# Kernel optimization log

Measured on AMD Instinct MI355X. Metric: run time of the kernel, lower is better.

## Reference

```python
import jax, jax.numpy as jnp
import numpy as np

HEAD_NUM = 16


def setup_inputs() -> dict:
    key = jax.random.key(0)
    ks = jax.random.split(key, 7)
    B, S, D = 4, 2048, 1024
    scale = 1.0 / np.sqrt(D)
    return {
        "q": jax.random.normal(ks[0], (B, S, D), jnp.float32),
        "k": jax.random.normal(ks[1], (B, S, D), jnp.float32),
        "v": jax.random.normal(ks[2], (B, S, D), jnp.float32),
        "w_q": jax.random.normal(ks[3], (D, D), jnp.float32) * scale,
        "w_k": jax.random.normal(ks[4], (D, D), jnp.float32) * scale,
        "w_v": jax.random.normal(ks[5], (D, D), jnp.float32) * scale,
        "w_o": jax.random.normal(ks[6], (D, D), jnp.float32) * scale,
    }


def reference(q, k, v, w_q, w_k, w_v, w_o):
    B, Sq, _ = q.shape
    H = HEAD_NUM
    d_k = w_q.shape[1] // H  # per-head key dim

    def split_heads(x):
        b, s, _ = x.shape
        return x.reshape(b, s, H, -1).transpose(0, 2, 1, 3)  # [b,h,s,d]

    hq = split_heads(q @ w_q)
    hk = split_heads(k @ w_k)
    hv = split_heads(v @ w_v)

    scores = jnp.einsum("bhqd,bhkd->bhqk", hq, hk) / jnp.sqrt(
        jnp.asarray(d_k, dtype=hq.dtype)
    )
    attn = jax.nn.softmax(scores, axis=-1)
    out = jnp.einsum("bhqk,bhkd->bhqd", attn, hv)  # [b,h,q,d]
    out = out.transpose(0, 2, 1, 3).reshape(B, Sq, -1)  # concat heads
    return out @ w_o
```

## Files before the change

kernel.cpp:

```cpp
#include <hip/hip_runtime.h>

typedef unsigned short u16;
typedef short vshort8 __attribute__((ext_vector_type(8)));
typedef __bf16 vbf16x8 __attribute__((ext_vector_type(8)));
typedef float vf32x4 __attribute__((ext_vector_type(4)));
typedef float vf32x16 __attribute__((ext_vector_type(16)));

__device__ __forceinline__ u16 f2bf(float f) {
  unsigned u = __builtin_bit_cast(unsigned, f);
  u += 0x7FFFu + ((u >> 16) & 1u);
  return (u16)(u >> 16);
}

__device__ __forceinline__ unsigned cvtpk(float lo, float hi) {
  unsigned r;
  asm("v_cvt_pk_bf16_f32 %0, %1, %2" : "=v"(r) : "v"(lo), "v"(hi));
  return r;
}

__device__ __forceinline__ void plswap(unsigned& a, unsigned& b) {
  asm("v_permlane32_swap_b32 %0, %1" : "+v"(a), "+v"(b));
}

__device__ __forceinline__ float swap32f(float x) { return __shfl_xor(x, 32); }

__device__ __forceinline__ vf32x4 mfma_bf16(vshort8 a, vshort8 b, vf32x4 c) {
  return __builtin_amdgcn_mfma_f32_16x16x32_bf16(
      __builtin_bit_cast(vbf16x8, a), __builtin_bit_cast(vbf16x8, b), c, 0, 0, 0);
}

__device__ __forceinline__ vf32x16 mfma32(vshort8 a, vshort8 b, vf32x16 c) {
  return __builtin_amdgcn_mfma_f32_32x32x16_bf16(
      __builtin_bit_cast(vbf16x8, a), __builtin_bit_cast(vbf16x8, b), c, 0, 0, 0);
}

__device__ __forceinline__ void gload16(const void* g, void* l) {
  __builtin_amdgcn_global_load_lds(
      (const __attribute__((address_space(1))) void*)g,
      (__attribute__((address_space(3))) void*)l, 16, 0, 0);
}

__global__ __launch_bounds__(256) void cvtk2(const float* __restrict__ a,
                                             const float* __restrict__ b,
                                             u16* __restrict__ oa,
                                             u16* __restrict__ ob, int n4) {
  const float* in = blockIdx.y ? b : a;
  u16* out = blockIdx.y ? ob : oa;
  if (in == nullptr) return;
  int idx = blockIdx.x * 256 + threadIdx.x;
  int stride = gridDim.x * 256;
  for (int i = idx; i < n4; i += stride) {
    float4 v = ((const float4*)in)[i];
    unsigned lo = (unsigned)f2bf(v.x) | ((unsigned)f2bf(v.y) << 16);
    unsigned hi = (unsigned)f2bf(v.z) | ((unsigned)f2bf(v.w) << 16);
    uint2 o; o.x = lo; o.y = hi;
    *(uint2*)&out[(size_t)i * 4] = o;
  }
}

__global__ __launch_bounds__(256) void wtrans4(const float* __restrict__ w0,
                                               const float* __restrict__ w1,
                                               const float* __restrict__ w2,
                                               const float* __restrict__ w3,
                                               u16* __restrict__ o0, u16* __restrict__ o1,
                                               u16* __restrict__ o2, u16* __restrict__ o3) {
  int z = blockIdx.z;
  const float* W = z == 0 ? w0 : z == 1 ? w1 : z == 2 ? w2 : w3;
  u16* Wt = z == 0 ? o0 : z == 1 ? o1 : z == 2 ? o2 : o3;
  __shared__ u16 tile[64][72];
  int t = threadIdx.x;
  int n0 = blockIdx.x * 64, k0 = blockIdx.y * 64;
#pragma unroll
  for (int it = 0; it < 4; ++it) {
    int cid = it * 256 + t;
    int r = cid >> 4, c4 = cid & 15;
    float4 v = *(const float4*)&W[(k0 + r) * 1024 + n0 + c4 * 4];
    u16* d = &tile[r][c4 * 4];
    d[0] = f2bf(v.x); d[1] = f2bf(v.y); d[2] = f2bf(v.z); d[3] = f2bf(v.w);
  }
  __syncthreads();
#pragma unroll
  for (int it = 0; it < 4; ++it) {
    int cid = it * 256 + t;
    int rn = cid >> 4, c4 = cid & 15;
    unsigned lo = (unsigned)tile[c4 * 4 + 0][rn] | ((unsigned)tile[c4 * 4 + 1][rn] << 16);
    unsigned hi = (unsigned)tile[c4 * 4 + 2][rn] | ((unsigned)tile[c4 * 4 + 3][rn] << 16);
    uint2 o; o.x = lo; o.y = hi;
    *(uint2*)&Wt[(n0 + rn) * 1024 + k0 + c4 * 4] = o;
  }
}

__global__ __launch_bounds__(256) void vtrans(const u16* __restrict__ V,
                                              u16* __restrict__ Vt) {
  __shared__ u16 tile[64][72];
  int t = threadIdx.x;
  int s0 = blockIdx.x * 64;
  int bh = blockIdx.y, b = bh >> 4, h = bh & 15;
#pragma unroll
  for (int it = 0; it < 2; ++it) {
    int cid = it * 256 + t;
    int r = cid >> 3, c8 = cid & 7;
    vshort8 v = *(const vshort8*)&V[(size_t)(b * 2048 + s0 + r) * 1024 + h * 64 + c8 * 8];
    *(vshort8*)&tile[r][c8 * 8] = v;
  }
  __syncthreads();
#pragma unroll
  for (int it = 0; it < 2; ++it) {
    int cid = it * 256 + t;
    int rd = cid >> 3, c8 = cid & 7;
    unsigned w[4];
#pragma unroll
    for (int j = 0; j < 4; ++j) {
      unsigned lo = tile[c8 * 8 + 2 * j][rd];
      unsigned hi = tile[c8 * 8 + 2 * j + 1][rd];
      w[j] = lo | (hi << 16);
    }
    uint4 o; o.x = w[0]; o.y = w[1]; o.z = w[2]; o.w = w[3];
    *(uint4*)&Vt[(size_t)(bh * 64 + rd) * 2048 + s0 + c8 * 8] = o;
  }
}

template <int OUTF32>
__device__ __forceinline__ void gemm_core(const u16* __restrict__ A,
                                          const u16* __restrict__ Bt,
                                          float* __restrict__ Cf,
                                          u16* __restrict__ Cb,
                                          int M, int N, int K, float oscale) {
  __shared__ __align__(16) u16 As[128 * 64];
  __shared__ __align__(16) u16 Bs[128 * 64];
  int t = threadIdx.x, lane = t & 63, wid = t >> 6;
  int g = lane >> 4, i16 = lane & 15;
  int n0 = blockIdx.x * 128, m0 = blockIdx.y * 128;
  int wm = wid >> 1, wn = wid & 1;

  vf32x4 acc[4][4];
#pragma unroll
  for (int a = 0; a < 4; ++a)
#pragma unroll
    for (int b = 0; b < 4; ++b) acc[a][b] = (vf32x4){0.f, 0.f, 0.f, 0.f};

  int ldsbase = (wid * 64) * 8;
  for (int kt = 0; kt < K / 64; ++kt) {
    if (kt) __syncthreads();
#pragma unroll
    for (int it = 0; it < 4; ++it) {
      int cid = it * 256 + t;
      int row = cid >> 3, c = cid & 7, sc = c ^ (row & 7);
      gload16(A + (size_t)(m0 + row) * K + kt * 64 + sc * 8, &As[it * 2048 + ldsbase]);
    }
#pragma unroll
    for (int it = 0; it < 4; ++it) {
      int cid = it * 256 + t;
      int row = cid >> 3, c = cid & 7, sc = c ^ (row & 7);
      gload16(Bt + (size_t)(n0 + row) * K + kt * 64 + sc * 8, &Bs[it * 2048 + ldsbase]);
    }
    __syncthreads();
#pragma unroll
    for (int kc = 0; kc < 2; ++kc) {
      vshort8 af[4], bf[4];
#pragma unroll
      for (int mf = 0; mf < 4; ++mf) {
        int row = wm * 64 + mf * 16 + i16;
        int ch = (kc * 4 + g) ^ (row & 7);
        af[mf] = *(const vshort8*)&As[row * 64 + ch * 8];
      }
#pragma unroll
      for (int nf = 0; nf < 4; ++nf) {
        int row = wn * 64 + nf * 16 + i16;
        int ch = (kc * 4 + g) ^ (row & 7);
        bf[nf] = *(const vshort8*)&Bs[row * 64 + ch * 8];
      }
#pragma unroll
      for (int mf = 0; mf < 4; ++mf)
#pragma unroll
        for (int nf = 0; nf < 4; ++nf)
          acc[mf][nf] = mfma_bf16(af[mf], bf[nf], acc[mf][nf]);
    }
  }
#pragma unroll
  for (int mf = 0; mf < 4; ++mf)
#pragma unroll
    for (int nf = 0; nf < 4; ++nf)
#pragma unroll
      for (int r = 0; r < 4; ++r) {
        int m = m0 + wm * 64 + mf * 16 + g * 4 + r;
        int n = n0 + wn * 64 + nf * 16 + i16;
        if (OUTF32)
          Cf[(size_t)m * N + n] = acc[mf][nf][r] * oscale;
        else
          Cb[(size_t)m * N + n] = f2bf(acc[mf][nf][r] * oscale);
      }
}

template <int OUTF32>
__global__ __launch_bounds__(256) void gemm_nt(const u16* __restrict__ A,
                                               const u16* __restrict__ Bt,
                                               float* __restrict__ Cf,
                                               u16* __restrict__ Cb,
                                               int M, int N, int K, float oscale) {
  gemm_core<OUTF32>(A, Bt, Cf, Cb, M, N, K, oscale);
}

__global__ __launch_bounds__(256) void gemm_nt2(const u16* __restrict__ A0,
                                                const u16* __restrict__ B0,
                                                u16* __restrict__ C0, float os0,
                                                const u16* __restrict__ A1,
                                                const u16* __restrict__ B1,
                                                u16* __restrict__ C1, float os1,
                                                int M, int N, int K) {
  if (blockIdx.z == 0)
    gemm_core<0>(A0, B0, nullptr, C0, M, N, K, os0);
  else
    gemm_core<0>(A1, B1, nullptr, C1, M, N, K, os1);
}

__device__ __forceinline__ void attn_body(int kt, const u16* __restrict__ Kbase,
                                          const u16* __restrict__ Vbase,
                                          vshort8 (&kfc)[2][4], vshort8 (&kfn)[2][4],
                                          vshort8 (&qf)[2][4], vf32x16 (&oacc)[2][2],
                                          float (&mrun)[2], float (&lrun)[2],
                                          int l31, int hi) {
  int ktn = kt + 1 < 32 ? kt + 1 : 31;
#pragma unroll
  for (int ks = 0; ks < 2; ++ks)
#pragma unroll
    for (int dc = 0; dc < 4; ++dc)
      kfn[ks][dc] = *(const vshort8*)&Kbase[(size_t)(ktn * 64 + ks * 32 + l31) * 1024 + dc * 16 + hi * 8];

  unsigned pk[2][2][8];
#pragma unroll
  for (int fq = 0; fq < 2; ++fq) {
    vf32x16 sacc[2];
#pragma unroll
    for (int ks = 0; ks < 2; ++ks)
#pragma unroll
      for (int r = 0; r < 16; ++r) sacc[ks][r] = 0.f;
    __builtin_amdgcn_s_setprio(1);
#pragma unroll
    for (int dc = 0; dc < 4; ++dc)
#pragma unroll
      for (int ks = 0; ks < 2; ++ks)
        sacc[ks] = mfma32(kfc[ks][dc], qf[fq][dc], sacc[ks]);
    __builtin_amdgcn_s_setprio(0);

    float tm[8];
#pragma unroll
    for (int r = 0; r < 8; ++r)
      tm[r] = fmaxf(fmaxf(sacc[0][r], sacc[0][r + 8]), fmaxf(sacc[1][r], sacc[1][r + 8]));
#pragma unroll
    for (int r = 0; r < 4; ++r) tm[r] = fmaxf(tm[r], tm[r + 4]);
    float pmax = fmaxf(fmaxf(tm[0], tm[1]), fmaxf(tm[2], tm[3]));
    pmax = fmaxf(pmax, swap32f(pmax));

    if (pmax > mrun[fq] + 8.f) {
      float al = exp2f(mrun[fq] - pmax);
      lrun[fq] *= al;
#pragma unroll
      for (int dm = 0; dm < 2; ++dm)
#pragma unroll
        for (int r = 0; r < 16; ++r) oacc[dm][fq][r] *= al;
      mrun[fq] = pmax;
    }
    float mm = mrun[fq];

    float s0 = 0.f, s1 = 0.f, s2 = 0.f, s3 = 0.f;
#pragma unroll
    for (int ks = 0; ks < 2; ++ks)
#pragma unroll
      for (int u = 0; u < 8; ++u) {
        float p0 = exp2f(sacc[ks][2 * u] - mm);
        float p1 = exp2f(sacc[ks][2 * u + 1] - mm);
        pk[fq][ks][u] = cvtpk(p0, p1);
        if (u & 1) { s0 += p0; s1 += p1; } else { s2 += p0; s3 += p1; }
      }
    lrun[fq] += (s0 + s1) + (s2 + s3);
  }

  vshort8 vtf[2][4];
#pragma unroll
  for (int dm = 0; dm < 2; ++dm)
#pragma unroll
    for (int s = 0; s < 4; ++s)
      vtf[dm][s] = *(const vshort8*)&Vbase[(size_t)(dm * 32 + l31) * 2048 + kt * 64 + s * 16 + hi * 8];

#pragma unroll
  for (int s = 0; s < 4; ++s) {
    vshort8 pb[2];
    const int ks = s >> 1, s1b = s & 1;
#pragma unroll
    for (int fq = 0; fq < 2; ++fq) {
      unsigned x0 = pk[fq][ks][4 * s1b + 0], x1 = pk[fq][ks][4 * s1b + 1];
      unsigned y0 = pk[fq][ks][4 * s1b + 2], y1 = pk[fq][ks][4 * s1b + 3];
      plswap(x0, y0);
      plswap(x1, y1);
      uint4 wv; wv.x = x0; wv.y = x1; wv.z = y0; wv.w = y1;
      pb[fq] = __builtin_bit_cast(vshort8, wv);
    }
    __builtin_amdgcn_s_setprio(1);
#pragma unroll
    for (int dm = 0; dm < 2; ++dm)
#pragma unroll
      for (int fq = 0; fq < 2; ++fq)
        oacc[dm][fq] = mfma32(vtf[dm][s], pb[fq], oacc[dm][fq]);
    __builtin_amdgcn_s_setprio(0);
  }
}

__global__ __launch_bounds__(512, 2) void attn_fwd9(const u16* __restrict__ Q,
                                                    const u16* __restrict__ K,
                                                    const u16* __restrict__ Vt,
                                                    u16* __restrict__ O) {
  int t = threadIdx.x, lane = t & 63, w = t >> 6;
  int l31 = lane & 31, hi = lane >> 5;
  int i = blockIdx.x;
  int qb = (i >> 3) & 3;
  int bh = (i & 7) + 8 * (i >> 5);
  int b = bh >> 4, h = bh & 15;

  const u16* Qbase = Q + (size_t)(b * 2048 + qb * 512 + w * 64) * 1024 + h * 64;
  const u16* Kbase = K + (size_t)(b * 2048) * 1024 + h * 64;
  const u16* Vbase = Vt + (size_t)(bh * 64) * 2048;

  vshort8 qf[2][4];
#pragma unroll
  for (int fq = 0; fq < 2; ++fq)
#pragma unroll
    for (int dc = 0; dc < 4; ++dc)
      qf[fq][dc] = *(const vshort8*)&Qbase[(size_t)(fq * 32 + l31) * 1024 + dc * 16 + hi * 8];

  vf32x16 oacc[2][2];
#pragma unroll
  for (int dm = 0; dm < 2; ++dm)
#pragma unroll
    for (int fq = 0; fq < 2; ++fq)
#pragma unroll
      for (int r = 0; r < 16; ++r) oacc[dm][fq][r] = 0.f;
  float mrun[2] = {-3.0e38f, -3.0e38f}, lrun[2] = {0.f, 0.f};

  vshort8 kfA[2][4], kfB[2][4];
#pragma unroll
  for (int ks = 0; ks < 2; ++ks)
#pragma unroll
    for (int dc = 0; dc < 4; ++dc)
      kfA[ks][dc] = *(const vshort8*)&Kbase[(size_t)(ks * 32 + l31) * 1024 + dc * 16 + hi * 8];

  for (int kt = 0; kt < 32; kt += 2) {
    attn_body(kt,     Kbase, Vbase, kfA, kfB, qf, oacc, mrun, lrun, l31, hi);
    attn_body(kt + 1, Kbase, Vbase, kfB, kfA, qf, oacc, mrun, lrun, l31, hi);
  }

#pragma unroll
  for (int fq = 0; fq < 2; ++fq) {
    float lt = lrun[fq] + swap32f(lrun[fq]);
    float inv = 1.f / lt;
    size_t qrow = (size_t)(b * 2048 + qb * 512 + w * 64 + fq * 32 + l31);
#pragma unroll
    for (int dm = 0; dm < 2; ++dm)
#pragma unroll
      for (int u = 0; u < 4; ++u) {
        unsigned w0 = cvtpk(oacc[dm][fq][4 * u + 0] * inv, oacc[dm][fq][4 * u + 1] * inv);
        unsigned w1 = cvtpk(oacc[dm][fq][4 * u + 2] * inv, oacc[dm][fq][4 * u + 3] * inv);
        uint2 o; o.x = w0; o.y = w1;
        *(uint2*)&O[qrow * 1024 + h * 64 + dm * 32 + 8 * u + 4 * hi] = o;
      }
  }
}

extern "C" void kernel_launch(void* const* d_in, const int* in_sizes, int n_in,
                              void* d_out, int out_size, void* d_ws, size_t ws_size,
                              hipStream_t stream) {
  const float* q  = (const float*)d_in[0];
  const float* k  = (const float*)d_in[1];
  const float* v  = (const float*)d_in[2];
  const float* wq = (const float*)d_in[3];
  const float* wk = (const float*)d_in[4];
  const float* wv = (const float*)d_in[5];
  const float* wo = (const float*)d_in[6];
  float* out = (float*)d_out;

  const int M = 8192, D = 1024;
  u16* Qb = (u16*)d_out;
  u16* Kb = Qb + (size_t)M * D;
  u16* xb  = (u16*)d_ws;
  u16* Vb  = xb + (size_t)M * D;
  u16* Vtg = Vb + (size_t)M * D;
  u16* wqt = Vtg + (size_t)M * D;
  u16* wkt = wqt + (size_t)D * D;
  u16* wvt = wkt + (size_t)D * D;
  u16* wot = wvt + (size_t)D * D;

  dim3 blk(256);
  wtrans4<<<dim3(16, 16, 4), blk, 0, stream>>>(wq, wk, wv, wo, wqt, wkt, wvt, wot);

  const float QSCALE = 0.125f * 1.44269504088896f;
  int n4 = M * D / 4;
  cvtk2<<<dim3(1024, 2), blk, 0, stream>>>(q, k, xb, Vtg, n4);
  gemm_nt2<<<dim3(8, 64, 2), blk, 0, stream>>>(xb, wqt, Qb, QSCALE,
                                               Vtg, wkt, Kb, 1.0f, M, D, D);
  cvtk2<<<dim3(1024, 1), blk, 0, stream>>>(v, nullptr, xb, nullptr, n4);
  gemm_nt<0><<<dim3(8, 64), blk, 0, stream>>>(xb, wvt, nullptr, Vb, M, D, D, 1.0f);

  vtrans<<<dim3(32, 64), blk, 0, stream>>>(Vb, Vtg);
  attn_fwd9<<<dim3(256), dim3(512), 0, stream>>>(Qb, Kb, Vtg, xb );
  gemm_nt<1><<<dim3(8, 64), blk, 0, stream>>>(xb, wot, out, nullptr, M, D, D, 1.0f);
}
```

Before: 265.8 us.

## Fuse fp32-to-bf16 input conversion into a single batched QKV projection GEMM

Removes the separate cvtk2 conversion kernels. The QKV GEMM now reads fp32 activations directly and packs them to bf16 with v_cvt_pk_bf16_f32 before storing into LDS. The Q, K and V projections are merged into one launch with a z-dimension of 3, and the output GEMM becomes a dedicated f32-output kernel. This drops the intermediate bf16 write/read traffic and several launches. In exchange, the A-tile load becomes a synchronous register round-trip instead of an async global_load_lds, and each fp32 A tile is fetched by all eight N-blocks at twice the byte size.

```diff
diff --git a/kernel.cpp b/kernel.cpp
--- a/kernel.cpp
+++ b/kernel.cpp
@@ -38,24 +38,6 @@
   __builtin_amdgcn_global_load_lds(
       (const __attribute__((address_space(1))) void*)g,
       (__attribute__((address_space(3))) void*)l, 16, 0, 0);
-}
-
-__global__ __launch_bounds__(256) void cvtk2(const float* __restrict__ a,
-                                             const float* __restrict__ b,
-                                             u16* __restrict__ oa,
-                                             u16* __restrict__ ob, int n4) {
-  const float* in = blockIdx.y ? b : a;
-  u16* out = blockIdx.y ? ob : oa;
-  if (in == nullptr) return;
-  int idx = blockIdx.x * 256 + threadIdx.x;
-  int stride = gridDim.x * 256;
-  for (int i = idx; i < n4; i += stride) {
-    float4 v = ((const float4*)in)[i];
-    unsigned lo = (unsigned)f2bf(v.x) | ((unsigned)f2bf(v.y) << 16);
-    unsigned hi = (unsigned)f2bf(v.z) | ((unsigned)f2bf(v.w) << 16);
-    uint2 o; o.x = lo; o.y = hi;
-    *(uint2*)&out[(size_t)i * 4] = o;
-  }
 }
 
 __global__ __launch_bounds__(256) void wtrans4(const float* __restrict__ w0,
@@ -120,12 +102,10 @@
   }
 }
 
-template <int OUTF32>
-__device__ __forceinline__ void gemm_core(const u16* __restrict__ A,
-                                          const u16* __restrict__ Bt,
-                                          float* __restrict__ Cf,
-                                          u16* __restrict__ Cb,
-                                          int M, int N, int K, float oscale) {
+__device__ __forceinline__ void gemm_core_f32A(const float* __restrict__ A,
+                                               const u16* __restrict__ Bt,
+                                               u16* __restrict__ Cb,
+                                               int M, int N, int K, float oscale) {
   __shared__ __align__(16) u16 As[128 * 64];
   __shared__ __align__(16) u16 Bs[128 * 64];
   int t = threadIdx.x, lane = t & 63, wid = t >> 6;
@@ -146,7 +126,13 @@
     for (int it = 0; it < 4; ++it) {
       int cid = it * 256 + t;
       int row = cid >> 3, c = cid & 7, sc = c ^ (row & 7);
-      gload16(A + (size_t)(m0 + row) * K + kt * 64 + sc * 8, &As[it * 2048 + ldsbase]);
+      const float* src = &A[(size_t)(m0 + row) * K + kt * 64 + sc * 8];
+      float4 v0 = *(const float4*)src;
+      float4 v1 = *(const float4*)(src + 4);
+      uint4 p;
+      p.x = cvtpk(v0.x, v0.y); p.y = cvtpk(v0.z, v0.w);
+      p.z = cvtpk(v1.x, v1.y); p.w = cvtpk(v1.z, v1.w);
+      *(uint4*)&As[cid * 8] = p;
     }
 #pragma unroll
     for (int it = 0; it < 4; ++it) {
@@ -185,33 +171,90 @@
       for (int r = 0; r < 4; ++r) {
         int m = m0 + wm * 64 + mf * 16 + g * 4 + r;
         int n = n0 + wn * 64 + nf * 16 + i16;
-        if (OUTF32)
-          Cf[(size_t)m * N + n] = acc[mf][nf][r] * oscale;
-        else
-          Cb[(size_t)m * N + n] = f2bf(acc[mf][nf][r] * oscale);
-      }
-}
-
-template <int OUTF32>
-__global__ __launch_bounds__(256) void gemm_nt(const u16* __restrict__ A,
+        Cb[(size_t)m * N + n] = f2bf(acc[mf][nf][r] * oscale);
+      }
+}
+
+__global__ __launch_bounds__(256) void gemm_qkv(const float* __restrict__ q,
+                                                const float* __restrict__ k,
+                                                const float* __restrict__ v,
+                                                const u16* __restrict__ wqt,
+                                                const u16* __restrict__ wkt,
+                                                const u16* __restrict__ wvt,
+                                                u16* __restrict__ Qb, u16* __restrict__ Kb,
+                                                u16* __restrict__ Vb, float qs) {
+  int z = blockIdx.z;
+  const float* A = z == 0 ? q : z == 1 ? k : v;
+  const u16* B = z == 0 ? wqt : z == 1 ? wkt : wvt;
+  u16* C = z == 0 ? Qb : z == 1 ? Kb : Vb;
+  gemm_core_f32A(A, B, C, 8192, 1024, 1024, z == 0 ? qs : 1.0f);
+}
+
+__global__ __launch_bounds__(256) void gemm_wo(const u16* __restrict__ A,
                                                const u16* __restrict__ Bt,
                                                float* __restrict__ Cf,
-                                               u16* __restrict__ Cb,
-                                               int M, int N, int K, float oscale) {
-  gemm_core<OUTF32>(A, Bt, Cf, Cb, M, N, K, oscale);
-}
-
-__global__ __launch_bounds__(256) void gemm_nt2(const u16* __restrict__ A0,
-                                                const u16* __restrict__ B0,
-                                                u16* __restrict__ C0, float os0,
-                                                const u16* __restrict__ A1,
-                                                const u16* __restrict__ B1,
-                                                u16* __restrict__ C1, float os1,
-                                                int M, int N, int K) {
-  if (blockIdx.z == 0)
-    gemm_core<0>(A0, B0, nullptr, C0, M, N, K, os0);
-  else
-    gemm_core<0>(A1, B1, nullptr, C1, M, N, K, os1);
+                                               int M, int N, int K) {
+  __shared__ __align__(16) u16 As[128 * 64];
+  __shared__ __align__(16) u16 Bs[128 * 64];
+  int t = threadIdx.x, lane = t & 63, wid = t >> 6;
+  int g = lane >> 4, i16 = lane & 15;
+  int n0 = blockIdx.x * 128, m0 = blockIdx.y * 128;
+  int wm = wid >> 1, wn = wid & 1;
+
+  vf32x4 acc[4][4];
+#pragma unroll
+  for (int a = 0; a < 4; ++a)
+#pragma unroll
+    for (int b = 0; b < 4; ++b) acc[a][b] = (vf32x4){0.f, 0.f, 0.f, 0.f};
+
+  int ldsbase = (wid * 64) * 8;
+  for (int kt = 0; kt < K / 64; ++kt) {
+    if (kt) __syncthreads();
+#pragma unroll
+    for (int it = 0; it < 4; ++it) {
+      int cid = it * 256 + t;
+      int row = cid >> 3, c = cid & 7, sc = c ^ (row & 7);
+      gload16(A + (size_t)(m0 + row) * K + kt * 64 + sc * 8, &As[it * 2048 + ldsbase]);
+    }
+#pragma unroll
+    for (int it = 0; it < 4; ++it) {
+      int cid = it * 256 + t;
+      int row = cid >> 3, c = cid & 7, sc = c ^ (row & 7);
+      gload16(Bt + (size_t)(n0 + row) * K + kt * 64 + sc * 8, &Bs[it * 2048 + ldsbase]);
+    }
+    __syncthreads();
+#pragma unroll
+    for (int kc = 0; kc < 2; ++kc) {
+      vshort8 af[4], bf[4];
+#pragma unroll
+      for (int mf = 0; mf < 4; ++mf) {
+        int row = wm * 64 + mf * 16 + i16;
+        int ch = (kc * 4 + g) ^ (row & 7);
+        af[mf] = *(const vshort8*)&As[row * 64 + ch * 8];
+      }
+#pragma unroll
+      for (int nf = 0; nf < 4; ++nf) {
+        int row = wn * 64 + nf * 16 + i16;
+        int ch = (kc * 4 + g) ^ (row & 7);
+        bf[nf] = *(const vshort8*)&Bs[row * 64 + ch * 8];
+      }
+#pragma unroll
+      for (int mf = 0; mf < 4; ++mf)
+#pragma unroll
+        for (int nf = 0; nf < 4; ++nf)
+          acc[mf][nf] = mfma_bf16(af[mf], bf[nf], acc[mf][nf]);
+    }
+  }
+#pragma unroll
+  for (int mf = 0; mf < 4; ++mf)
+#pragma unroll
+    for (int nf = 0; nf < 4; ++nf)
+#pragma unroll
+      for (int r = 0; r < 4; ++r) {
+        int m = m0 + wm * 64 + mf * 16 + g * 4 + r;
+        int n = n0 + wn * 64 + nf * 16 + i16;
+        Cf[(size_t)m * N + n] = acc[mf][nf][r];
+      }
 }
 
 __device__ __forceinline__ void attn_body(int kt, const u16* __restrict__ Kbase,
@@ -393,14 +436,9 @@
   wtrans4<<<dim3(16, 16, 4), blk, 0, stream>>>(wq, wk, wv, wo, wqt, wkt, wvt, wot);
 
   const float QSCALE = 0.125f * 1.44269504088896f;
-  int n4 = M * D / 4;
-  cvtk2<<<dim3(1024, 2), blk, 0, stream>>>(q, k, xb, Vtg, n4);
-  gemm_nt2<<<dim3(8, 64, 2), blk, 0, stream>>>(xb, wqt, Qb, QSCALE,
-                                               Vtg, wkt, Kb, 1.0f, M, D, D);
-  cvtk2<<<dim3(1024, 1), blk, 0, stream>>>(v, nullptr, xb, nullptr, n4);
-  gemm_nt<0><<<dim3(8, 64), blk, 0, stream>>>(xb, wvt, nullptr, Vb, M, D, D, 1.0f);
+  gemm_qkv<<<dim3(8, 64, 3), blk, 0, stream>>>(q, k, v, wqt, wkt, wvt, Qb, Kb, Vb, QSCALE);
 
   vtrans<<<dim3(32, 64), blk, 0, stream>>>(Vb, Vtg);
   attn_fwd9<<<dim3(256), dim3(512), 0, stream>>>(Qb, Kb, Vtg, xb );
-  gemm_nt<1><<<dim3(8, 64), blk, 0, stream>>>(xb, wot, out, nullptr, M, D, D, 1.0f);
-}
+  gemm_wo<<<dim3(8, 64), blk, 0, stream>>>(xb, wot, out, M, D, D);
+}
```

Measured after the change: 286.2 us. 7.7% more time.
